# Performance work log

Measured on AMD Instinct MI355X. Metric: run time of the kernel, lower is better.

The kernel has to match this reference:

```python
import jax, jax.numpy as jnp
import numpy as np

TARGET_DIM, DRUG_DIM, INT_DIM, HID = 1024, 128, 128, 32
LN_EPS = 1e-5  # torch nn.LayerNorm default (module's eps arg is unused for LN)


def _layernorm(x, g, b):
    mu = jnp.mean(x, axis=-1, keepdims=True)
    var = jnp.var(x, axis=-1, keepdims=True)
    return (x - mu) * jax.lax.rsqrt(var + LN_EPS) * g + b


def setup_inputs() -> dict:
    key = jax.random.key(0)
    ks = jax.random.split(key, 10)
    B, NR, NA = 4, 512, 64
    s_t = 1.0 / np.sqrt(TARGET_DIM)
    s_d = 1.0 / np.sqrt(DRUG_DIM)
    s_o = 1.0 / np.sqrt(HID * HID)
    return {
        "target_embedding": jax.random.normal(ks[0], (B, NR, TARGET_DIM), jnp.float32),
        "drug_embedding": jax.random.normal(ks[1], (B, NA, DRUG_DIM), jnp.float32),
        "target_mask": jnp.ones((B, NR), jnp.float32),
        "drug_mask": jnp.ones((B, NA), jnp.float32),
        "ln_t_g": jnp.ones((TARGET_DIM,), jnp.float32),
        "ln_t_b": jnp.zeros((TARGET_DIM,), jnp.float32),
        "ln_d_g": jnp.ones((DRUG_DIM,), jnp.float32),
        "ln_d_b": jnp.zeros((DRUG_DIM,), jnp.float32),
        "W_t": jax.random.uniform(ks[2], (HID, TARGET_DIM), jnp.float32, -s_t, s_t),
        "b_t": jax.random.uniform(ks[3], (HID,), jnp.float32, -s_t, s_t),
        "W_d": jax.random.uniform(ks[4], (HID, DRUG_DIM), jnp.float32, -s_d, s_d),
        "b_d": jax.random.uniform(ks[5], (HID,), jnp.float32, -s_d, s_d),
        "W_out": jax.random.uniform(ks[6], (INT_DIM, HID * HID), jnp.float32, -s_o, s_o),
        "b_out": jax.random.uniform(ks[7], (INT_DIM,), jnp.float32, -s_o, s_o),
    }


def reference(target_embedding, drug_embedding, target_mask, drug_mask,
              ln_t_g, ln_t_b, ln_d_g, ln_d_b, W_t, b_t, W_d, b_d, W_out, b_out):
    t = _layernorm(target_embedding, ln_t_g, ln_t_b)
    d = _layernorm(drug_embedding, ln_d_g, ln_d_b)
    # projections + mask: [B,NR,H], [B,NA,H]
    tf = (t @ W_t.T + b_t) * target_mask[..., None]
    df = (d @ W_d.T + b_d) * drug_mask[..., None]
    # fused outer-product + linear_out: W_out row index i over flat (c*H+e)
    W3 = W_out.reshape(INT_DIM, HID, HID)  # [i, c, e]
    outer = jnp.einsum('bnc,bme,ice->bnmi', tf, df, W3) + b_out
    mask = target_mask[:, :, None] * drug_mask[:, None, :]  # [B,NR,NA]
    outer = outer * mask[..., None]
    return outer, mask
```

## Files before the change

### kernel.cpp

```cpp
#include <hip/hip_runtime.h>

typedef __attribute__((ext_vector_type(8))) short short8;
typedef __attribute__((ext_vector_type(4))) float f32x4;

#define YSTR 1032
#define GSTR 1048

__device__ __forceinline__ unsigned short f2bf(float f) {
  union { float f; unsigned u; } v; v.f = f;
  unsigned r = v.u + 0x7FFFu + ((v.u >> 16) & 1u);
  return (unsigned short)(r >> 16);
}
__device__ __forceinline__ unsigned pack2(float a, float b) {
  return (unsigned)f2bf(a) | ((unsigned)f2bf(b) << 16);
}
__device__ __forceinline__ short8 packW(float4 a, float4 b) {
  union { short8 s; unsigned u[4]; } r;
  r.u[0] = pack2(a.x, a.y); r.u[1] = pack2(a.z, a.w);
  r.u[2] = pack2(b.x, b.y); r.u[3] = pack2(b.z, b.w);
  return r.s;
}

template<int ROWLEN>
__device__ __forceinline__ void lnproj8(
    const float* __restrict__ X, const float* __restrict__ g, const float* __restrict__ bia,
    const float* __restrict__ W, const float* __restrict__ pb, const float* __restrict__ msk,
    unsigned short* __restrict__ outb, int row0, unsigned short* Yl, float* pd, int tid)
{
  const int w = tid >> 6, lid = tid & 63, l = tid & 15, q = (tid >> 4) & 3;

  #pragma unroll
  for (int rr = 0; rr < 2; ++rr) {
    const int row = w * 2 + rr;
    const float* xr = X + (size_t)(row0 + row) * ROWLEN;
    if (ROWLEN == 1024) {
      float4 v[4];
      float s = 0.f, s2 = 0.f;
      #pragma unroll
      for (int k = 0; k < 4; ++k) {
        v[k] = *(const float4*)(xr + 4 * lid + 256 * k);
        s  += (v[k].x + v[k].y) + (v[k].z + v[k].w);
        s2 += (v[k].x * v[k].x + v[k].y * v[k].y) + (v[k].z * v[k].z + v[k].w * v[k].w);
      }
      #pragma unroll
      for (int off = 32; off >= 1; off >>= 1) { s += __shfl_xor(s, off, 64); s2 += __shfl_xor(s2, off, 64); }
      const float mu = s * (1.f / 1024.f);
      const float rs = rsqrtf(s2 * (1.f / 1024.f) - mu * mu + 1e-5f);
      #pragma unroll
      for (int k = 0; k < 4; ++k) {
        float4 gg = *(const float4*)(g + 4 * lid + 256 * k);
        float4 bb = *(const float4*)(bia + 4 * lid + 256 * k);
        unsigned* yd = (unsigned*)(Yl + row * YSTR + 4 * lid + 256 * k);
        yd[0] = pack2((v[k].x - mu) * rs * gg.x + bb.x, (v[k].y - mu) * rs * gg.y + bb.y);
        yd[1] = pack2((v[k].z - mu) * rs * gg.z + bb.z, (v[k].w - mu) * rs * gg.w + bb.w);
      }
    } else {
      float2 v = *(const float2*)(xr + 2 * lid);
      float s = v.x + v.y, s2 = v.x * v.x + v.y * v.y;
      #pragma unroll
      for (int off = 32; off >= 1; off >>= 1) { s += __shfl_xor(s, off, 64); s2 += __shfl_xor(s2, off, 64); }
      const float mu = s * (1.f / 128.f);
      const float rs = rsqrtf(s2 * (1.f / 128.f) - mu * mu + 1e-5f);
      float2 gg = *(const float2*)(g + 2 * lid);
      float2 bb = *(const float2*)(bia + 2 * lid);
      *(unsigned*)(Yl + row * YSTR + 2 * lid) =
          pack2((v.x - mu) * rs * gg.x + bb.x, (v.y - mu) * rs * gg.y + bb.y);
    }
  }
  __syncthreads();

  const int KST = ROWLEN / 32;
  const int ht = w & 1, kh = w >> 1;
  const int h = ht * 16 + l;
  f32x4 acc = {0.f, 0.f, 0.f, 0.f};
  #pragma unroll
  for (int s = kh * (KST / 2); s < kh * (KST / 2) + KST / 2; ++s) {
    short8 af = *(const short8*)(Yl + l * YSTR + s * 32 + q * 8);
    const float* wp = W + (size_t)h * ROWLEN + s * 32 + q * 8;
    short8 bf = packW(*(const float4*)wp, *(const float4*)(wp + 4));
    acc = __builtin_amdgcn_mfma_f32_16x16x32_bf16(af, bf, acc, 0, 0, 0);
  }
  if (kh == 1 && q < 2) {
    #pragma unroll
    for (int r = 0; r < 4; ++r) pd[ht * 128 + (q * 4 + r) * 16 + l] = acc[r];
  }
  __syncthreads();
  if (kh == 0 && q < 2) {
    const float pbv = pb[h];
    #pragma unroll
    for (int r = 0; r < 4; ++r) {
      const int rl = q * 4 + r, rg = row0 + rl;
      float val = acc[r] + pd[ht * 128 + rl * 16 + l] + pbv;
      outb[(size_t)rg * 32 + h] = f2bf(val * msk[rg]);
    }
  }
}

__global__ __launch_bounds__(256) void k_pre(
    const float* __restrict__ tgt, const float* __restrict__ drg,
    const float* __restrict__ tmask, const float* __restrict__ dmask,
    const float* __restrict__ ln_t_g, const float* __restrict__ ln_t_b,
    const float* __restrict__ ln_d_g, const float* __restrict__ ln_d_b,
    const float* __restrict__ W_t, const float* __restrict__ b_t,
    const float* __restrict__ W_d, const float* __restrict__ b_d,
    const float* __restrict__ W_out,
    unsigned short* __restrict__ w3pp, unsigned short* __restrict__ tfb,
    unsigned short* __restrict__ dfb)
{
  __shared__ unsigned short Yl[16 * YSTR];
  __shared__ float pd[2 * 8 * 16];
  const int blk = blockIdx.x, tid = threadIdx.x;
  if (blk < 256) {
    lnproj8<1024>(tgt, ln_t_g, ln_t_b, W_t, b_t, tmask, tfb, blk * 8, Yl, pd, tid);
  } else if (blk < 288) {
    lnproj8<128>(drg, ln_d_g, ln_d_b, W_d, b_d, dmask, dfb, (blk - 256) * 8, Yl, pd, tid);
  } else {
    const int f = (blk - 288) * 256 + tid;
    const int i = f >> 5, e = f & 31;
    unsigned short us[32];
    #pragma unroll
    for (int c = 0; c < 32; ++c) us[c] = f2bf(W_out[i * 1024 + c * 32 + e]);
    unsigned* dst = (unsigned*)(w3pp + (size_t)f * 32);
    #pragma unroll
    for (int j = 0; j < 16; ++j) dst[j] = (unsigned)us[2 * j] | ((unsigned)us[2 * j + 1] << 16);
  }
}

__global__ __launch_bounds__(256) void k_main(
    const unsigned short* __restrict__ w3pp, const unsigned short* __restrict__ tfb,
    const unsigned short* __restrict__ dfb, const float* __restrict__ b_out,
    const float* __restrict__ tmask, const float* __restrict__ dmask,
    float* __restrict__ out, float* __restrict__ mask_out)
{
  __shared__ unsigned short Gl[16 * GSTR];
  const int id = blockIdx.x;
  const int b = id >> 7, n16 = (id >> 2) & 31, iq = id & 3;
  const int n0 = n16 * 16, i0 = iq * 32;
  const int tid = threadIdx.x, w = tid >> 6, l = tid & 15, q = (tid >> 4) & 3;

  short8 atf = *(const short8*)(tfb + (size_t)(b * 512 + n0 + l) * 32 + q * 8);
  short8 bdf[4];
  #pragma unroll
  for (int mt = 0; mt < 4; ++mt)
    bdf[mt] = *(const short8*)(dfb + (size_t)(b * 64 + mt * 16 + l) * 32 + q * 8);

  const f32x4 zero = {0.f, 0.f, 0.f, 0.f};

  #pragma unroll 8
  for (int t = 0; t < 16; ++t) {
    const int tt = w * 16 + t;
    short8 bw = *(const short8*)(w3pp + (size_t)(i0 * 32 + tt * 16 + l) * 32 + q * 8);
    f32x4 d = __builtin_amdgcn_mfma_f32_16x16x32_bf16(atf, bw, zero, 0, 0, 0);
    const int floc = tt * 16 + l, ip = floc >> 5, e = floc & 31;
    #pragma unroll
    for (int r = 0; r < 4; ++r)
      Gl[(q * 4 + r) * GSTR + ip * 32 + e] = f2bf(d[r]);
  }
  __syncthreads();

  const float4 bo0 = *(const float4*)(b_out + i0 + q * 4);
  const float4 bo1 = *(const float4*)(b_out + i0 + 16 + q * 4);
  float dm[4];
  #pragma unroll
  for (int mt = 0; mt < 4; ++mt) dm[mt] = dmask[b * 64 + mt * 16 + l];

  for (int j = 0; j < 8; ++j) {
    const int p = w * 8 + j, n = p >> 1, it = p & 1;
    short8 ag = *(const short8*)(Gl + n * GSTR + (it * 16 + l) * 32 + q * 8);
    const float tmv = tmask[b * 512 + n0 + n];
    const float4 bo = it ? bo1 : bo0;
    const size_t obase = ((size_t)(b * 512 + n0 + n) * 64) * 128 + (size_t)(i0 + it * 16 + q * 4);
    #pragma unroll
    for (int mt = 0; mt < 4; ++mt) {
      f32x4 d = __builtin_amdgcn_mfma_f32_16x16x32_bf16(ag, bdf[mt], zero, 0, 0, 0);
      const float s = tmv * dm[mt];
      float4 o;
      o.x = (d[0] + bo.x) * s; o.y = (d[1] + bo.y) * s;
      o.z = (d[2] + bo.z) * s; o.w = (d[3] + bo.w) * s;
      *(float4*)(out + obase + (size_t)(mt * 16 + l) * 128) = o;
    }
  }

  if (iq == 0) {
    #pragma unroll
    for (int k = 0; k < 4; ++k) {
      const int t = tid + k * 256;
      const int n = t >> 6, m = t & 63;
      mask_out[(size_t)(b * 512 + n0 + n) * 64 + m] =
          tmask[b * 512 + n0 + n] * dmask[b * 64 + m];
    }
  }
}

extern "C" void kernel_launch(void* const* d_in, const int* in_sizes, int n_in,
                              void* d_out, int out_size, void* d_ws, size_t ws_size,
                              hipStream_t stream)
{
  const float* tgt    = (const float*)d_in[0];
  const float* drg    = (const float*)d_in[1];
  const float* tmask  = (const float*)d_in[2];
  const float* dmask  = (const float*)d_in[3];
  const float* ln_t_g = (const float*)d_in[4];
  const float* ln_t_b = (const float*)d_in[5];
  const float* ln_d_g = (const float*)d_in[6];
  const float* ln_d_b = (const float*)d_in[7];
  const float* W_t    = (const float*)d_in[8];
  const float* b_t    = (const float*)d_in[9];
  const float* W_d    = (const float*)d_in[10];
  const float* b_d    = (const float*)d_in[11];
  const float* W_out  = (const float*)d_in[12];
  const float* b_out  = (const float*)d_in[13];

  float* out = (float*)d_out;
  float* mask_out = out + (size_t)4 * 512 * 64 * 128;

  char* ws = (char*)d_ws;
  unsigned short* w3pp = (unsigned short*)(ws);
  unsigned short* tfb  = (unsigned short*)(ws + 262144);
  unsigned short* dfb  = (unsigned short*)(ws + 262144 + 131072);

  k_pre<<<dim3(304), dim3(256), 0, stream>>>(
      tgt, drg, tmask, dmask, ln_t_g, ln_t_b, ln_d_g, ln_d_b,
      W_t, b_t, W_d, b_d, W_out, w3pp, tfb, dfb);
  k_main<<<dim3(512), dim3(256), 0, stream>>>(
      w3pp, tfb, dfb, b_out, tmask, dmask, out, mask_out);
}
```

Baseline: 119.6 us.

## Fuse preprocessing into main kernel, recomputing projections per block

Merges the LayerNorm/projection pre-kernel and the main outer-product kernel into one launch. Each block now computes its own 16 target rows' LN and projection, redundantly recomputes the whole batch's drug LN and projection, and reads and converts W_out from fp32 directly instead of from a pre-packed bf16 workspace. This removes one launch, the inter-kernel dependency and the workspace round trip. In exchange, every block repeats drug and W_out work (each target tile is redone by 4 blocks) and issues strided uncoalesced fp32 W_out loads.

```diff
diff --git a/kernel.cpp b/kernel.cpp
--- a/kernel.cpp
+++ b/kernel.cpp
@@ -5,6 +5,9 @@
 
 #define YSTR 1032
 #define GSTR 1048
+#define TFS  40
+#define DFYS 132
+#define DFBS 40
 
 __device__ __forceinline__ unsigned short f2bf(float f) {
   union { float f; unsigned u; } v; v.f = f;
@@ -21,152 +24,162 @@
   return r.s;
 }
 
-template<int ROWLEN>
-__device__ __forceinline__ void lnproj8(
-    const float* __restrict__ X, const float* __restrict__ g, const float* __restrict__ bia,
-    const float* __restrict__ W, const float* __restrict__ pb, const float* __restrict__ msk,
-    unsigned short* __restrict__ outb, int row0, unsigned short* Yl, float* pd, int tid)
-{
-  const int w = tid >> 6, lid = tid & 63, l = tid & 15, q = (tid >> 4) & 3;
-
-  #pragma unroll
-  for (int rr = 0; rr < 2; ++rr) {
-    const int row = w * 2 + rr;
-    const float* xr = X + (size_t)(row0 + row) * ROWLEN;
-    if (ROWLEN == 1024) {
-      float4 v[4];
-      float s = 0.f, s2 = 0.f;
-      #pragma unroll
-      for (int k = 0; k < 4; ++k) {
-        v[k] = *(const float4*)(xr + 4 * lid + 256 * k);
-        s  += (v[k].x + v[k].y) + (v[k].z + v[k].w);
-        s2 += (v[k].x * v[k].x + v[k].y * v[k].y) + (v[k].z * v[k].z + v[k].w * v[k].w);
-      }
-      #pragma unroll
-      for (int off = 32; off >= 1; off >>= 1) { s += __shfl_xor(s, off, 64); s2 += __shfl_xor(s2, off, 64); }
-      const float mu = s * (1.f / 1024.f);
-      const float rs = rsqrtf(s2 * (1.f / 1024.f) - mu * mu + 1e-5f);
-      #pragma unroll
-      for (int k = 0; k < 4; ++k) {
-        float4 gg = *(const float4*)(g + 4 * lid + 256 * k);
-        float4 bb = *(const float4*)(bia + 4 * lid + 256 * k);
-        unsigned* yd = (unsigned*)(Yl + row * YSTR + 4 * lid + 256 * k);
-        yd[0] = pack2((v[k].x - mu) * rs * gg.x + bb.x, (v[k].y - mu) * rs * gg.y + bb.y);
-        yd[1] = pack2((v[k].z - mu) * rs * gg.z + bb.z, (v[k].w - mu) * rs * gg.w + bb.w);
-      }
-    } else {
-      float2 v = *(const float2*)(xr + 2 * lid);
-      float s = v.x + v.y, s2 = v.x * v.x + v.y * v.y;
-      #pragma unroll
-      for (int off = 32; off >= 1; off >>= 1) { s += __shfl_xor(s, off, 64); s2 += __shfl_xor(s2, off, 64); }
-      const float mu = s * (1.f / 128.f);
-      const float rs = rsqrtf(s2 * (1.f / 128.f) - mu * mu + 1e-5f);
-      float2 gg = *(const float2*)(g + 2 * lid);
-      float2 bb = *(const float2*)(bia + 2 * lid);
-      *(unsigned*)(Yl + row * YSTR + 2 * lid) =
-          pack2((v.x - mu) * rs * gg.x + bb.x, (v.y - mu) * rs * gg.y + bb.y);
-    }
-  }
-  __syncthreads();
-
-  const int KST = ROWLEN / 32;
-  const int ht = w & 1, kh = w >> 1;
-  const int h = ht * 16 + l;
-  f32x4 acc = {0.f, 0.f, 0.f, 0.f};
-  #pragma unroll
-  for (int s = kh * (KST / 2); s < kh * (KST / 2) + KST / 2; ++s) {
-    short8 af = *(const short8*)(Yl + l * YSTR + s * 32 + q * 8);
-    const float* wp = W + (size_t)h * ROWLEN + s * 32 + q * 8;
-    short8 bf = packW(*(const float4*)wp, *(const float4*)(wp + 4));
-    acc = __builtin_amdgcn_mfma_f32_16x16x32_bf16(af, bf, acc, 0, 0, 0);
-  }
-  if (kh == 1 && q < 2) {
-    #pragma unroll
-    for (int r = 0; r < 4; ++r) pd[ht * 128 + (q * 4 + r) * 16 + l] = acc[r];
-  }
-  __syncthreads();
-  if (kh == 0 && q < 2) {
-    const float pbv = pb[h];
-    #pragma unroll
-    for (int r = 0; r < 4; ++r) {
-      const int rl = q * 4 + r, rg = row0 + rl;
-      float val = acc[r] + pd[ht * 128 + rl * 16 + l] + pbv;
-      outb[(size_t)rg * 32 + h] = f2bf(val * msk[rg]);
-    }
-  }
-}
-
-__global__ __launch_bounds__(256) void k_pre(
+__global__ __launch_bounds__(256) void k_fused(
     const float* __restrict__ tgt, const float* __restrict__ drg,
     const float* __restrict__ tmask, const float* __restrict__ dmask,
     const float* __restrict__ ln_t_g, const float* __restrict__ ln_t_b,
     const float* __restrict__ ln_d_g, const float* __restrict__ ln_d_b,
     const float* __restrict__ W_t, const float* __restrict__ b_t,
     const float* __restrict__ W_d, const float* __restrict__ b_d,
-    const float* __restrict__ W_out,
-    unsigned short* __restrict__ w3pp, unsigned short* __restrict__ tfb,
-    unsigned short* __restrict__ dfb)
-{
-  __shared__ unsigned short Yl[16 * YSTR];
-  __shared__ float pd[2 * 8 * 16];
-  const int blk = blockIdx.x, tid = threadIdx.x;
-  if (blk < 256) {
-    lnproj8<1024>(tgt, ln_t_g, ln_t_b, W_t, b_t, tmask, tfb, blk * 8, Yl, pd, tid);
-  } else if (blk < 288) {
-    lnproj8<128>(drg, ln_d_g, ln_d_b, W_d, b_d, dmask, dfb, (blk - 256) * 8, Yl, pd, tid);
-  } else {
-    const int f = (blk - 288) * 256 + tid;
-    const int i = f >> 5, e = f & 31;
-    unsigned short us[32];
-    #pragma unroll
-    for (int c = 0; c < 32; ++c) us[c] = f2bf(W_out[i * 1024 + c * 32 + e]);
-    unsigned* dst = (unsigned*)(w3pp + (size_t)f * 32);
-    #pragma unroll
-    for (int j = 0; j < 16; ++j) dst[j] = (unsigned)us[2 * j] | ((unsigned)us[2 * j + 1] << 16);
-  }
-}
-
-__global__ __launch_bounds__(256) void k_main(
-    const unsigned short* __restrict__ w3pp, const unsigned short* __restrict__ tfb,
-    const unsigned short* __restrict__ dfb, const float* __restrict__ b_out,
-    const float* __restrict__ tmask, const float* __restrict__ dmask,
+    const float* __restrict__ W_out, const float* __restrict__ b_out,
     float* __restrict__ out, float* __restrict__ mask_out)
 {
-  __shared__ unsigned short Gl[16 * GSTR];
+  __shared__ union { unsigned short Yl[16 * YSTR]; unsigned short Gl[16 * GSTR]; } U1;
+  __shared__ union { float pd[3 * 2 * 16 * 16]; unsigned short DFy[64 * DFYS]; } U2;
+  __shared__ unsigned short TFl[16 * TFS];
+  __shared__ unsigned short DFb[64 * DFBS];
+
   const int id = blockIdx.x;
   const int b = id >> 7, n16 = (id >> 2) & 31, iq = id & 3;
   const int n0 = n16 * 16, i0 = iq * 32;
-  const int tid = threadIdx.x, w = tid >> 6, l = tid & 15, q = (tid >> 4) & 3;
-
-  short8 atf = *(const short8*)(tfb + (size_t)(b * 512 + n0 + l) * 32 + q * 8);
-  short8 bdf[4];
+  const int tid = threadIdx.x, w = tid >> 6, lid = tid & 63, l = tid & 15, q = (tid >> 4) & 3;
+  const f32x4 zero = {0.f, 0.f, 0.f, 0.f};
+
   #pragma unroll
-  for (int mt = 0; mt < 4; ++mt)
-    bdf[mt] = *(const short8*)(dfb + (size_t)(b * 64 + mt * 16 + l) * 32 + q * 8);
-
-  const f32x4 zero = {0.f, 0.f, 0.f, 0.f};
-
-  #pragma unroll 8
-  for (int t = 0; t < 16; ++t) {
-    const int tt = w * 16 + t;
-    short8 bw = *(const short8*)(w3pp + (size_t)(i0 * 32 + tt * 16 + l) * 32 + q * 8);
-    f32x4 d = __builtin_amdgcn_mfma_f32_16x16x32_bf16(atf, bw, zero, 0, 0, 0);
-    const int floc = tt * 16 + l, ip = floc >> 5, e = floc & 31;
-    #pragma unroll
-    for (int r = 0; r < 4; ++r)
-      Gl[(q * 4 + r) * GSTR + ip * 32 + e] = f2bf(d[r]);
+  for (int rr = 0; rr < 4; ++rr) {
+    const int row = w * 4 + rr;
+    const float* xr = tgt + (size_t)(b * 512 + n0 + row) * 1024;
+    float4 v[4];
+    float s = 0.f, s2 = 0.f;
+    #pragma unroll
+    for (int k = 0; k < 4; ++k) {
+      v[k] = *(const float4*)(xr + 4 * lid + 256 * k);
+      s  += (v[k].x + v[k].y) + (v[k].z + v[k].w);
+      s2 += (v[k].x * v[k].x + v[k].y * v[k].y) + (v[k].z * v[k].z + v[k].w * v[k].w);
+    }
+    #pragma unroll
+    for (int off = 32; off >= 1; off >>= 1) { s += __shfl_xor(s, off, 64); s2 += __shfl_xor(s2, off, 64); }
+    const float mu = s * (1.f / 1024.f);
+    const float rs = rsqrtf(s2 * (1.f / 1024.f) - mu * mu + 1e-5f);
+    #pragma unroll
+    for (int k = 0; k < 4; ++k) {
+      float4 gg = *(const float4*)(ln_t_g + 4 * lid + 256 * k);
+      float4 bb = *(const float4*)(ln_t_b + 4 * lid + 256 * k);
+      unsigned* yd = (unsigned*)(U1.Yl + row * YSTR + 4 * lid + 256 * k);
+      yd[0] = pack2((v[k].x - mu) * rs * gg.x + bb.x, (v[k].y - mu) * rs * gg.y + bb.y);
+      yd[1] = pack2((v[k].z - mu) * rs * gg.z + bb.z, (v[k].w - mu) * rs * gg.w + bb.w);
+    }
+  }
+  __syncthreads();
+
+  f32x4 acc0 = zero, acc1 = zero;
+  #pragma unroll
+  for (int ss = 0; ss < 8; ++ss) {
+    const int s = w * 8 + ss;
+    short8 af = *(const short8*)(U1.Yl + l * YSTR + s * 32 + q * 8);
+    const float* wp0 = W_t + (size_t)l * 1024 + s * 32 + q * 8;
+    const float* wp1 = W_t + (size_t)(16 + l) * 1024 + s * 32 + q * 8;
+    acc0 = __builtin_amdgcn_mfma_f32_16x16x32_bf16(af, packW(*(const float4*)wp0, *(const float4*)(wp0 + 4)), acc0, 0, 0, 0);
+    acc1 = __builtin_amdgcn_mfma_f32_16x16x32_bf16(af, packW(*(const float4*)wp1, *(const float4*)(wp1 + 4)), acc1, 0, 0, 0);
+  }
+  if (w > 0) {
+    #pragma unroll
+    for (int r = 0; r < 4; ++r) {
+      U2.pd[(w - 1) * 512 + (q * 4 + r) * 16 + l]       = acc0[r];
+      U2.pd[(w - 1) * 512 + 256 + (q * 4 + r) * 16 + l] = acc1[r];
+    }
+  }
+  __syncthreads();
+
+  if (w == 0) {
+    #pragma unroll
+    for (int ht = 0; ht < 2; ++ht) {
+      const int h = ht * 16 + l;
+      const float pbv = b_t[h];
+      #pragma unroll
+      for (int r = 0; r < 4; ++r) {
+        const int rl = q * 4 + r;
+        float val = (ht ? acc1[r] : acc0[r]) + pbv;
+        #pragma unroll
+        for (int k = 0; k < 3; ++k) val += U2.pd[k * 512 + ht * 256 + rl * 16 + l];
+        val *= tmask[b * 512 + n0 + rl];
+        TFl[rl * TFS + h] = f2bf(val);
+      }
+    }
+  }
+  __syncthreads();
+
+  for (int rr = 0; rr < 16; ++rr) {
+    const int m = w * 16 + rr;
+    const float* xr = drg + (size_t)(b * 64 + m) * 128;
+    float2 v = *(const float2*)(xr + 2 * lid);
+    float s = v.x + v.y, s2 = v.x * v.x + v.y * v.y;
+    #pragma unroll
+    for (int off = 32; off >= 1; off >>= 1) { s += __shfl_xor(s, off, 64); s2 += __shfl_xor(s2, off, 64); }
+    const float mu = s * (1.f / 128.f);
+    const float rs = rsqrtf(s2 * (1.f / 128.f) - mu * mu + 1e-5f);
+    float2 gg = *(const float2*)(ln_d_g + 2 * lid);
+    float2 bb = *(const float2*)(ln_d_b + 2 * lid);
+    *(unsigned*)(U2.DFy + m * DFYS + 2 * lid) =
+        pack2((v.x - mu) * rs * gg.x + bb.x, (v.y - mu) * rs * gg.y + bb.y);
+  }
+  __syncthreads();
+
+  {
+    f32x4 a0 = zero, a1 = zero;
+    #pragma unroll
+    for (int s = 0; s < 4; ++s) {
+      short8 af = *(const short8*)(U2.DFy + (w * 16 + l) * DFYS + s * 32 + q * 8);
+      const float* wp0 = W_d + (size_t)l * 128 + s * 32 + q * 8;
+      const float* wp1 = W_d + (size_t)(16 + l) * 128 + s * 32 + q * 8;
+      a0 = __builtin_amdgcn_mfma_f32_16x16x32_bf16(af, packW(*(const float4*)wp0, *(const float4*)(wp0 + 4)), a0, 0, 0, 0);
+      a1 = __builtin_amdgcn_mfma_f32_16x16x32_bf16(af, packW(*(const float4*)wp1, *(const float4*)(wp1 + 4)), a1, 0, 0, 0);
+    }
+    #pragma unroll
+    for (int ht = 0; ht < 2; ++ht) {
+      const int h = ht * 16 + l;
+      const float pbv = b_d[h];
+      #pragma unroll
+      for (int r = 0; r < 4; ++r) {
+        const int m = w * 16 + q * 4 + r;
+        float val = (ht ? a1[r] : a0[r]) + pbv;
+        val *= dmask[b * 64 + m];
+        DFb[m * DFBS + h] = f2bf(val);
+      }
+    }
+  }
+
+  {
+    short8 atf = *(const short8*)(TFl + l * TFS + q * 8);
+    for (int t = 0; t < 16; ++t) {
+      const int floc = (w * 16 + t) * 16 + l;
+      const int i = i0 + (floc >> 5), e = floc & 31;
+      const float* wp = W_out + (size_t)i * 1024 + q * 8 * 32 + e;
+      union { short8 s; unsigned u[4]; } bw;
+      #pragma unroll
+      for (int j = 0; j < 4; ++j)
+        bw.u[j] = pack2(wp[(2 * j) * 32], wp[(2 * j + 1) * 32]);
+      f32x4 d = __builtin_amdgcn_mfma_f32_16x16x32_bf16(atf, bw.s, zero, 0, 0, 0);
+      const int ip = floc >> 5, e2 = floc & 31;
+      #pragma unroll
+      for (int r = 0; r < 4; ++r)
+        U1.Gl[(q * 4 + r) * GSTR + ip * 32 + e2] = f2bf(d[r]);
+    }
   }
   __syncthreads();
 
   const float4 bo0 = *(const float4*)(b_out + i0 + q * 4);
   const float4 bo1 = *(const float4*)(b_out + i0 + 16 + q * 4);
+  short8 bdf[4];
   float dm[4];
   #pragma unroll
-  for (int mt = 0; mt < 4; ++mt) dm[mt] = dmask[b * 64 + mt * 16 + l];
-
+  for (int mt = 0; mt < 4; ++mt) {
+    bdf[mt] = *(const short8*)(DFb + (mt * 16 + l) * DFBS + q * 8);
+    dm[mt] = dmask[b * 64 + mt * 16 + l];
+  }
   for (int j = 0; j < 8; ++j) {
     const int p = w * 8 + j, n = p >> 1, it = p & 1;
-    short8 ag = *(const short8*)(Gl + n * GSTR + (it * 16 + l) * 32 + q * 8);
+    short8 ag = *(const short8*)(U1.Gl + n * GSTR + (it * 16 + l) * 32 + q * 8);
     const float tmv = tmask[b * 512 + n0 + n];
     const float4 bo = it ? bo1 : bo0;
     const size_t obase = ((size_t)(b * 512 + n0 + n) * 64) * 128 + (size_t)(i0 + it * 16 + q * 4);
@@ -214,14 +227,7 @@
   float* out = (float*)d_out;
   float* mask_out = out + (size_t)4 * 512 * 64 * 128;
 
-  char* ws = (char*)d_ws;
-  unsigned short* w3pp = (unsigned short*)(ws);
-  unsigned short* tfb  = (unsigned short*)(ws + 262144);
-  unsigned short* dfb  = (unsigned short*)(ws + 262144 + 131072);
-
-  k_pre<<<dim3(304), dim3(256), 0, stream>>>(
+  k_fused<<<dim3(512), dim3(256), 0, stream>>>(
       tgt, drg, tmask, dmask, ln_t_g, ln_t_b, ln_d_g, ln_d_b,
-      W_t, b_t, W_d, b_d, W_out, w3pp, tfb, dfb);
-  k_main<<<dim3(512), dim3(256), 0, stream>>>(
-      w3pp, tfb, dfb, b_out, tmask, dmask, out, mask_out);
-}
+      W_t, b_t, W_d, b_d, W_out, b_out, out, mask_out);
+}
```

Result: slower. 128.4 us (+7.4%).
